# Kernel optimization log

Hardware: AMD Instinct MI355X
Metric: run time of the kernel (lower is better)

## Reference

```python
import jax, jax.numpy as jnp
import numpy as np
from functools import partial

B, T = 2048, 500
H1, H2, D_IN, D_FC, N_CLS = 128, 64, 1, 128, 4

def _lstm_scan(x, Wih, Whh, bih, bhh, hidden, return_seq):
    # x: (B, T, D). PyTorch gate order: i, f, g, o. Weights: (4H, D) / (4H, H).
    Bsz = x.shape[0]
    b = bih + bhh
    xg = jnp.einsum('btd,gd->btg', x, Wih) + b  # precompute input projections (B,T,4H)
    xg = jnp.swapaxes(xg, 0, 1)                 # (T,B,4H)
    h0 = jnp.zeros((Bsz, hidden), x.dtype)
    c0 = jnp.zeros((Bsz, hidden), x.dtype)

    def step(carry, gt):
        h, c = carry
        gates = gt + h @ Whh.T
        i, f, g, o = jnp.split(gates, 4, axis=-1)
        c = jax.nn.sigmoid(f) * c + jax.nn.sigmoid(i) * jnp.tanh(g)
        h = jax.nn.sigmoid(o) * jnp.tanh(c)
        return (h, c), (h if return_seq else None)

    (hT, _), hs = jax.lax.scan(step, (h0, c0), xg)
    if return_seq:
        return jnp.swapaxes(hs, 0, 1)  # (B,T,H)
    return hT  # (B,H)

def setup_inputs() -> dict:
    key = jax.random.key(0)
    ks = jax.random.split(key, 16)
    n = lambda k, shape: jax.random.normal(k, shape, dtype=jnp.float32) * 0.05
    return {
        'x': jax.random.normal(ks[0], (B, 1, T), dtype=jnp.float32),
        'Wp': n(ks[1], (H1, D_IN)), 'bp': n(ks[2], (H1,)),
        'Wih1': n(ks[3], (4 * H1, H1)), 'Whh1': n(ks[4], (4 * H1, H1)),
        'bih1': n(ks[5], (4 * H1,)), 'bhh1': n(ks[6], (4 * H1,)),
        'Wih2': n(ks[7], (4 * H2, H1)), 'Whh2': n(ks[8], (4 * H2, H2)),
        'bih2': n(ks[9], (4 * H2,)), 'bhh2': n(ks[10], (4 * H2,)),
        'W1': n(ks[11], (D_FC, H2)), 'b1': n(ks[12], (D_FC,)),
        'W2': n(ks[13], (N_CLS, D_FC)), 'b2': n(ks[14], (N_CLS,)),
    }

def reference(x, Wp, bp, Wih1, Whh1, bih1, bhh1, Wih2, Whh2, bih2, bhh2, W1, b1, W2, b2):
    # x: (B,1,T) -> (B,T,1)
    h = jnp.swapaxes(x, 1, 2)
    h = h @ Wp.T + bp                                         # (B,T,128)
    h = _lstm_scan(h, Wih1, Whh1, bih1, bhh1, H1, True)       # (B,T,128); dropout is identity in eval
    h = _lstm_scan(h, Wih2, Whh2, bih2, bhh2, H2, False)      # (B,64) == last-timestep output
    h = jax.nn.relu(h @ W1.T + b1)                            # (B,128)
    return h @ W2.T + b2                                      # (B,4)
```

## Files before the change

### kernel.cpp

```cpp
#include <hip/hip_runtime.h>


#define B_   2048
#define T_   500
#define BM   8
#define NBLK (B_ / BM)
#define NTHR 768

typedef __attribute__((ext_vector_type(8))) short bf16x8;
typedef __attribute__((ext_vector_type(4))) float f32x4;

#define LOG2E 1.44269504088896340736f

static __device__ __forceinline__ short f2bf(float f) {
  unsigned u = __builtin_bit_cast(unsigned, f);
  u = (u + 0x7fffu + ((u >> 16) & 1u)) >> 16;
  return (short)u;
}

static __device__ __forceinline__ float lstm_cell_s(float gi, float gf, float gg,
                                                    float go, float& c) {
  float Ei = __builtin_amdgcn_exp2f(-gi);
  float Eg = __builtin_amdgcn_exp2f(gg + gg);
  float Ef = __builtin_amdgcn_exp2f(-gf);
  float Eo = __builtin_amdgcn_exp2f(-go);
  float t12 = (1.f + Ei) * (1.f + Eg);
  float num = c * t12 + (Eg - 1.f) * (1.f + Ef);
  c = num * __builtin_amdgcn_rcpf((1.f + Ef) * t12);
  float Ec = __builtin_amdgcn_exp2f(2.88539008177792681472f * c);
  return (Ec - 1.f) * __builtin_amdgcn_rcpf((1.f + Eo) * (1.f + Ec));
}

__global__ __launch_bounds__(NTHR)
void lstm_fused(const float* __restrict__ X,
                const float* __restrict__ Wp,
                const float* __restrict__ bp,
                const float* __restrict__ Wih1,
                const float* __restrict__ Whh1,
                const float* __restrict__ bih1,
                const float* __restrict__ bhh1,
                const float* __restrict__ Wih2,
                const float* __restrict__ Whh2,
                const float* __restrict__ bih2,
                const float* __restrict__ bhh2,
                const float* __restrict__ W1,
                const float* __restrict__ b1,
                const float* __restrict__ W2,
                const float* __restrict__ b2,
                float* __restrict__ Out) {
  __shared__ __align__(16) short h1b[2][16][136];
  __shared__ __align__(16) short h2b[2][16][72];
  __shared__ __align__(16) short w2h[4][4][2][64][8];
  __shared__ float h2f[8][64];
  __shared__ float fc1s[8][132];

  const int tid = threadIdx.x;
  const int ln = tid & 63;
  const int wv = tid >> 6;
  const int cl = ln & 15;
  const int kg = ln >> 4;
  const int r0 = blockIdx.x * BM;
  const bool isL1 = (wv >= 4);
  const int w1 = wv - 4;

  bf16x8 Wreg[4][4];
  float uv[8];

  if (isL1) {
#pragma unroll
    for (int n = 0; n < 4; ++n) {
      const int R = n * 128 + 16 * w1 + cl;
      float u = 0.f, vv = bih1[R] + bhh1[R];
      const float4* Wi4 = (const float4*)(Wih1 + R * 128);
      const float4* Wp4 = (const float4*)Wp;
      const float4* bp4 = (const float4*)bp;
#pragma unroll 4
      for (int d = 0; d < 32; ++d) {
        float4 a = Wi4[d], pw = Wp4[d], qb = bp4[d];
        u  += a.x*pw.x + a.y*pw.y + a.z*pw.z + a.w*pw.w;
        vv += a.x*qb.x + a.y*qb.y + a.z*qb.z + a.w*qb.w;
      }
      uv[n] = u * LOG2E;
      uv[4 + n] = vv * LOG2E;
#pragma unroll
      for (int kf = 0; kf < 4; ++kf) {
        const float4* s4 = (const float4*)(Whh1 + R * 128 + kf * 32 + kg * 8);
        float4 a0 = s4[0], a1 = s4[1];
        bf16x8 fr;
        fr[0]=f2bf(a0.x*LOG2E); fr[1]=f2bf(a0.y*LOG2E);
        fr[2]=f2bf(a0.z*LOG2E); fr[3]=f2bf(a0.w*LOG2E);
        fr[4]=f2bf(a1.x*LOG2E); fr[5]=f2bf(a1.y*LOG2E);
        fr[6]=f2bf(a1.z*LOG2E); fr[7]=f2bf(a1.w*LOG2E);
        Wreg[n][kf] = fr;
      }
    }
  } else {
#pragma unroll
    for (int n = 0; n < 4; ++n) {
      const int R = n * 64 + 16 * wv + cl;
      uv[n] = (bih2[R] + bhh2[R]) * LOG2E;
#pragma unroll
      for (int kf = 0; kf < 4; ++kf) {
        const float4* s4 = (const float4*)(Wih2 + R * 128 + kf * 32 + kg * 8);
        float4 a0 = s4[0], a1 = s4[1];
        bf16x8 fr;
        fr[0]=f2bf(a0.x*LOG2E); fr[1]=f2bf(a0.y*LOG2E);
        fr[2]=f2bf(a0.z*LOG2E); fr[3]=f2bf(a0.w*LOG2E);
        fr[4]=f2bf(a1.x*LOG2E); fr[5]=f2bf(a1.y*LOG2E);
        fr[6]=f2bf(a1.z*LOG2E); fr[7]=f2bf(a1.w*LOG2E);
        Wreg[n][kf] = fr;
      }
#pragma unroll
      for (int kf = 0; kf < 2; ++kf) {
        const float4* s4 = (const float4*)(Whh2 + R * 64 + kf * 32 + kg * 8);
        float4 a0 = s4[0], a1 = s4[1];
        short* dst = &w2h[wv][n][kf][ln][0];
        dst[0]=f2bf(a0.x*LOG2E); dst[1]=f2bf(a0.y*LOG2E);
        dst[2]=f2bf(a0.z*LOG2E); dst[3]=f2bf(a0.w*LOG2E);
        dst[4]=f2bf(a1.x*LOG2E); dst[5]=f2bf(a1.y*LOG2E);
        dst[6]=f2bf(a1.z*LOG2E); dst[7]=f2bf(a1.w*LOG2E);
      }
    }
  }

  for (int i = tid; i < 2 * 16 * 136; i += NTHR) ((short*)h1b)[i] = 0;
  for (int i = tid; i < 2 * 16 * 72;  i += NTHR) ((short*)h2b)[i] = 0;
  __syncthreads();

  float c0 = 0.f, c1 = 0.f;
  const int rA = (kg < 2) ? kg * 4 : (kg - 2) * 4 + 2;
  const int rB = rA + 1;
  const int uu = 16 * (isL1 ? w1 : wv) + cl;

  float xr[4];
#pragma unroll
  for (int e = 0; e < 4; ++e)
    xr[e] = (isL1 && kg < 2) ? X[(size_t)(r0 + kg * 4 + e) * T_ + 0] : 0.f;

  for (int i = 0; i <= T_; ++i) {
    const int cur = i & 1, prv = cur ^ 1;

    if (isL1) {
      if (i < T_) {
        bf16x8 a1[4];
#pragma unroll
        for (int kf = 0; kf < 4; ++kf)
          a1[kf] = *(const bf16x8*)&h1b[prv][cl][kf * 32 + kg * 8];

        f32x4 acc[4];
#pragma unroll
        for (int n = 0; n < 4; ++n) {
#pragma unroll
          for (int e = 0; e < 4; ++e)
            acc[n][e] = xr[e] * uv[n] + uv[4 + n];
        }
        __builtin_amdgcn_s_setprio(1);
#pragma unroll
        for (int n = 0; n < 4; ++n)
#pragma unroll
          for (int kf = 0; kf < 4; ++kf)
            acc[n] = __builtin_amdgcn_mfma_f32_16x16x32_bf16(
                a1[kf], Wreg[n][kf], acc[n], 0, 0, 0);
        __builtin_amdgcn_s_setprio(0);

        if (kg < 2) {
          const int tn = (i + 1 < T_) ? i + 1 : T_ - 1;
#pragma unroll
          for (int e = 0; e < 4; ++e)
            xr[e] = X[(size_t)(r0 + kg * 4 + e) * T_ + tn];
        }

        float gA[4], gB[4];
#pragma unroll
        for (int n = 0; n < 4; ++n) {
          float s2 = __shfl_xor(acc[n][2], 32);
          float s3 = __shfl_xor(acc[n][3], 32);
          gA[n] = (kg < 2) ? acc[n][0] : s2;
          gB[n] = (kg < 2) ? acc[n][1] : s3;
        }
        float hA = lstm_cell_s(gA[0], gA[1], gA[2], gA[3], c0);
        float hB = lstm_cell_s(gB[0], gB[1], gB[2], gB[3], c1);
        h1b[cur][rA][uu] = f2bf(hA);
        h1b[cur][rB][uu] = f2bf(hB);
      }
    } else {
      if (i > 0) {
        bf16x8 a1[4], ag[2];
#pragma unroll
        for (int kf = 0; kf < 4; ++kf)
          a1[kf] = *(const bf16x8*)&h1b[prv][cl][kf * 32 + kg * 8];
#pragma unroll
        for (int kf = 0; kf < 2; ++kf)
          ag[kf] = *(const bf16x8*)&h2b[cur][cl][kf * 32 + kg * 8];

        f32x4 acc[4];
#pragma unroll
        for (int n = 0; n < 4; ++n)
          acc[n] = (f32x4){uv[n], uv[n], uv[n], uv[n]};
        __builtin_amdgcn_s_setprio(1);
#pragma unroll
        for (int n = 0; n < 4; ++n) {
          bf16x8 w0 = *(const bf16x8*)&w2h[wv][n][0][ln][0];
          bf16x8 w1f = *(const bf16x8*)&w2h[wv][n][1][ln][0];
          acc[n] = __builtin_amdgcn_mfma_f32_16x16x32_bf16(ag[0], w0, acc[n], 0, 0, 0);
          acc[n] = __builtin_amdgcn_mfma_f32_16x16x32_bf16(ag[1], w1f, acc[n], 0, 0, 0);
#pragma unroll
          for (int kf = 0; kf < 4; ++kf)
            acc[n] = __builtin_amdgcn_mfma_f32_16x16x32_bf16(
                a1[kf], Wreg[n][kf], acc[n], 0, 0, 0);
        }
        __builtin_amdgcn_s_setprio(0);

        float gA[4], gB[4];
#pragma unroll
        for (int n = 0; n < 4; ++n) {
          float s2 = __shfl_xor(acc[n][2], 32);
          float s3 = __shfl_xor(acc[n][3], 32);
          gA[n] = (kg < 2) ? acc[n][0] : s2;
          gB[n] = (kg < 2) ? acc[n][1] : s3;
        }
        float hA = lstm_cell_s(gA[0], gA[1], gA[2], gA[3], c0);
        float hB = lstm_cell_s(gB[0], gB[1], gB[2], gB[3], c1);
        h2b[prv][rA][uu] = f2bf(hA);
        h2b[prv][rB][uu] = f2bf(hB);
        if (i == T_) { h2f[rA][uu] = hA; h2f[rB][uu] = hB; }
      }
    }
    __syncthreads();
  }

  if (tid < 512) {
    const int u = tid & 127, r2 = tid >> 7;
    float a0 = b1[u], a1f = b1[u];
    for (int k = 0; k < 64; ++k) {
      float w = W1[u * 64 + k];
      a0  += h2f[r2 * 2 + 0][k] * w;
      a1f += h2f[r2 * 2 + 1][k] * w;
    }
    fc1s[r2 * 2 + 0][u] = fmaxf(a0, 0.f);
    fc1s[r2 * 2 + 1][u] = fmaxf(a1f, 0.f);
  }
  __syncthreads();
  if (tid < 32) {
    const int r = tid >> 2, cls = tid & 3;
    float a = b2[cls];
    for (int k = 0; k < 128; ++k) a += fc1s[r][k] * W2[cls * 128 + k];
    Out[(size_t)(r0 + r) * 4 + cls] = a;
  }
}

extern "C" void kernel_launch(void* const* d_in, const int* in_sizes, int n_in,
                              void* d_out, int out_size, void* d_ws, size_t ws_size,
                              hipStream_t stream) {
  const float* X    = (const float*)d_in[0];
  const float* Wp   = (const float*)d_in[1];
  const float* bp   = (const float*)d_in[2];
  const float* Wih1 = (const float*)d_in[3];
  const float* Whh1 = (const float*)d_in[4];
  const float* bih1 = (const float*)d_in[5];
  const float* bhh1 = (const float*)d_in[6];
  const float* Wih2 = (const float*)d_in[7];
  const float* Whh2 = (const float*)d_in[8];
  const float* bih2 = (const float*)d_in[9];
  const float* bhh2 = (const float*)d_in[10];
  const float* W1   = (const float*)d_in[11];
  const float* b1   = (const float*)d_in[12];
  const float* W2   = (const float*)d_in[13];
  const float* b2   = (const float*)d_in[14];
  float* Out = (float*)d_out;

  hipLaunchKernelGGL(lstm_fused, dim3(NBLK), dim3(NTHR), 0, stream,
                     X, Wp, bp, Wih1, Whh1, bih1, bhh1,
                     Wih2, Whh2, bih2, bhh2, W1, b1, W2, b2, Out);
}
```

Measured before the change: 534.8 us.

## Stage inputs in LDS, keep Whh2 in registers, peel loop edges, pack bf16 converts

Preloads the whole input sequence for the block's 8 rows into shared memory before the recurrence. This replaces the per-step global loads of X in layer-1 waves with one LDS vector read. Layer-2 recurrent weights move from LDS into registers, which removes two LDS reads per gate per step. The first and last timesteps are peeled out of the loop so the per-iteration branches disappear, and the two bf16 conversions are packed into one v_cvt_pk_bf16_f32. In exchange, register pressure rises in the layer-2 waves and the prologue pays a serialized global load into a 32 KB LDS buffer.

```diff
diff --git a/kernel.cpp b/kernel.cpp
--- a/kernel.cpp
+++ b/kernel.cpp
@@ -50,7 +50,7 @@
                 float* __restrict__ Out) {
   __shared__ __align__(16) short h1b[2][16][136];
   __shared__ __align__(16) short h2b[2][16][72];
-  __shared__ __align__(16) short w2h[4][4][2][64][8];
+  __shared__ __align__(16) float xs[T_][16];
   __shared__ float h2f[8][64];
   __shared__ float fc1s[8][132];
 
@@ -64,6 +64,7 @@
   const int w1 = wv - 4;
 
   bf16x8 Wreg[4][4];
+  bf16x8 W2h[4][2];
   float uv[8];
 
   if (isL1) {
@@ -114,17 +115,24 @@
       for (int kf = 0; kf < 2; ++kf) {
         const float4* s4 = (const float4*)(Whh2 + R * 64 + kf * 32 + kg * 8);
         float4 a0 = s4[0], a1 = s4[1];
-        short* dst = &w2h[wv][n][kf][ln][0];
-        dst[0]=f2bf(a0.x*LOG2E); dst[1]=f2bf(a0.y*LOG2E);
-        dst[2]=f2bf(a0.z*LOG2E); dst[3]=f2bf(a0.w*LOG2E);
-        dst[4]=f2bf(a1.x*LOG2E); dst[5]=f2bf(a1.y*LOG2E);
-        dst[6]=f2bf(a1.z*LOG2E); dst[7]=f2bf(a1.w*LOG2E);
+        bf16x8 fr;
+        fr[0]=f2bf(a0.x*LOG2E); fr[1]=f2bf(a0.y*LOG2E);
+        fr[2]=f2bf(a0.z*LOG2E); fr[3]=f2bf(a0.w*LOG2E);
+        fr[4]=f2bf(a1.x*LOG2E); fr[5]=f2bf(a1.y*LOG2E);
+        fr[6]=f2bf(a1.z*LOG2E); fr[7]=f2bf(a1.w*LOG2E);
+        W2h[n][kf] = fr;
       }
     }
   }
 
   for (int i = tid; i < 2 * 16 * 136; i += NTHR) ((short*)h1b)[i] = 0;
   for (int i = tid; i < 2 * 16 * 72;  i += NTHR) ((short*)h2b)[i] = 0;
+  for (int i = tid; i < T_ * 16; i += NTHR) ((float*)xs)[i] = 0.f;
+  __syncthreads();
+#pragma unroll
+  for (int r = 0; r < 8; ++r)
+    for (int t = tid; t < T_; t += NTHR)
+      xs[t][r] = X[(size_t)(r0 + r) * T_ + t];
   __syncthreads();
 
   float c0 = 0.f, c1 = 0.f;
@@ -132,102 +140,102 @@
   const int rB = rA + 1;
   const int uu = 16 * (isL1 ? w1 : wv) + cl;
 
-  float xr[4];
-#pragma unroll
-  for (int e = 0; e < 4; ++e)
-    xr[e] = (isL1 && kg < 2) ? X[(size_t)(r0 + kg * 4 + e) * T_ + 0] : 0.f;
-
-  for (int i = 0; i <= T_; ++i) {
+#define L1_STEP(i, cur, prv)                                                  \
+  {                                                                           \
+    bf16x8 a1[4];                                                             \
+    _Pragma("unroll")                                                         \
+    for (int kf = 0; kf < 4; ++kf)                                            \
+      a1[kf] = *(const bf16x8*)&h1b[prv][cl][kf * 32 + kg * 8];               \
+    f32x4 xr4 = *(const f32x4*)&xs[i][kg * 4];                                \
+    f32x4 acc[4];                                                             \
+    _Pragma("unroll")                                                         \
+    for (int n = 0; n < 4; ++n) {                                             \
+      _Pragma("unroll")                                                       \
+      for (int e = 0; e < 4; ++e)                                             \
+        acc[n][e] = xr4[e] * uv[n] + uv[4 + n];                               \
+    }                                                                         \
+    __builtin_amdgcn_s_setprio(1);                                            \
+    _Pragma("unroll")                                                         \
+    for (int n = 0; n < 4; ++n)                                               \
+      _Pragma("unroll")                                                       \
+      for (int kf = 0; kf < 4; ++kf)                                          \
+        acc[n] = __builtin_amdgcn_mfma_f32_16x16x32_bf16(                     \
+            a1[kf], Wreg[n][kf], acc[n], 0, 0, 0);                            \
+    __builtin_amdgcn_s_setprio(0);                                            \
+    float gA[4], gB[4];                                                       \
+    _Pragma("unroll")                                                         \
+    for (int n = 0; n < 4; ++n) {                                             \
+      float s2 = __shfl_xor(acc[n][2], 32);                                   \
+      float s3 = __shfl_xor(acc[n][3], 32);                                   \
+      gA[n] = (kg < 2) ? acc[n][0] : s2;                                      \
+      gB[n] = (kg < 2) ? acc[n][1] : s3;                                      \
+    }                                                                         \
+    float hA = lstm_cell_s(gA[0], gA[1], gA[2], gA[3], c0);                   \
+    float hB = lstm_cell_s(gB[0], gB[1], gB[2], gB[3], c1);                   \
+    unsigned pk;                                                              \
+    asm("v_cvt_pk_bf16_f32 %0, %1, %2" : "=v"(pk) : "v"(hA), "v"(hB));        \
+    h1b[cur][rA][uu] = (short)pk;                                             \
+    h1b[cur][rB][uu] = (short)(pk >> 16);                                     \
+  }
+
+#define L2_STEP(cur, prv, FINAL)                                              \
+  {                                                                           \
+    bf16x8 a1[4], ag[2];                                                      \
+    _Pragma("unroll")                                                         \
+    for (int kf = 0; kf < 4; ++kf)                                            \
+      a1[kf] = *(const bf16x8*)&h1b[prv][cl][kf * 32 + kg * 8];               \
+    _Pragma("unroll")                                                         \
+    for (int kf = 0; kf < 2; ++kf)                                            \
+      ag[kf] = *(const bf16x8*)&h2b[cur][cl][kf * 32 + kg * 8];               \
+    f32x4 acc[4];                                                             \
+    _Pragma("unroll")                                                         \
+    for (int n = 0; n < 4; ++n)                                               \
+      acc[n] = (f32x4){uv[n], uv[n], uv[n], uv[n]};                           \
+    __builtin_amdgcn_s_setprio(1);                                            \
+    _Pragma("unroll")                                                         \
+    for (int n = 0; n < 4; ++n) {                                             \
+      acc[n] = __builtin_amdgcn_mfma_f32_16x16x32_bf16(ag[0], W2h[n][0],      \
+                                                       acc[n], 0, 0, 0);      \
+      acc[n] = __builtin_amdgcn_mfma_f32_16x16x32_bf16(ag[1], W2h[n][1],      \
+                                                       acc[n], 0, 0, 0);      \
+      _Pragma("unroll")                                                       \
+      for (int kf = 0; kf < 4; ++kf)                                          \
+        acc[n] = __builtin_amdgcn_mfma_f32_16x16x32_bf16(                     \
+            a1[kf], Wreg[n][kf], acc[n], 0, 0, 0);                            \
+    }                                                                         \
+    __builtin_amdgcn_s_setprio(0);                                            \
+    float gA[4], gB[4];                                                       \
+    _Pragma("unroll")                                                         \
+    for (int n = 0; n < 4; ++n) {                                             \
+      float s2 = __shfl_xor(acc[n][2], 32);                                   \
+      float s3 = __shfl_xor(acc[n][3], 32);                                   \
+      gA[n] = (kg < 2) ? acc[n][0] : s2;                                      \
+      gB[n] = (kg < 2) ? acc[n][1] : s3;                                      \
+    }                                                                         \
+    float hA = lstm_cell_s(gA[0], gA[1], gA[2], gA[3], c0);                   \
+    float hB = lstm_cell_s(gB[0], gB[1], gB[2], gB[3], c1);                   \
+    unsigned pk;                                                              \
+    asm("v_cvt_pk_bf16_f32 %0, %1, %2" : "=v"(pk) : "v"(hA), "v"(hB));        \
+    h2b[prv][rA][uu] = (short)pk;                                             \
+    h2b[prv][rB][uu] = (short)(pk >> 16);                                     \
+    if (FINAL) { h2f[rA][uu] = hA; h2f[rB][uu] = hB; }                        \
+  }
+
+  if (isL1) L1_STEP(0, 0, 1);
+  __syncthreads();
+
+  for (int i = 1; i < T_; ++i) {
     const int cur = i & 1, prv = cur ^ 1;
-
     if (isL1) {
-      if (i < T_) {
-        bf16x8 a1[4];
-#pragma unroll
-        for (int kf = 0; kf < 4; ++kf)
-          a1[kf] = *(const bf16x8*)&h1b[prv][cl][kf * 32 + kg * 8];
-
-        f32x4 acc[4];
-#pragma unroll
-        for (int n = 0; n < 4; ++n) {
-#pragma unroll
-          for (int e = 0; e < 4; ++e)
-            acc[n][e] = xr[e] * uv[n] + uv[4 + n];
-        }
-        __builtin_amdgcn_s_setprio(1);
-#pragma unroll
-        for (int n = 0; n < 4; ++n)
-#pragma unroll
-          for (int kf = 0; kf < 4; ++kf)
-            acc[n] = __builtin_amdgcn_mfma_f32_16x16x32_bf16(
-                a1[kf], Wreg[n][kf], acc[n], 0, 0, 0);
-        __builtin_amdgcn_s_setprio(0);
-
-        if (kg < 2) {
-          const int tn = (i + 1 < T_) ? i + 1 : T_ - 1;
-#pragma unroll
-          for (int e = 0; e < 4; ++e)
-            xr[e] = X[(size_t)(r0 + kg * 4 + e) * T_ + tn];
-        }
-
-        float gA[4], gB[4];
-#pragma unroll
-        for (int n = 0; n < 4; ++n) {
-          float s2 = __shfl_xor(acc[n][2], 32);
-          float s3 = __shfl_xor(acc[n][3], 32);
-          gA[n] = (kg < 2) ? acc[n][0] : s2;
-          gB[n] = (kg < 2) ? acc[n][1] : s3;
-        }
-        float hA = lstm_cell_s(gA[0], gA[1], gA[2], gA[3], c0);
-        float hB = lstm_cell_s(gB[0], gB[1], gB[2], gB[3], c1);
-        h1b[cur][rA][uu] = f2bf(hA);
-        h1b[cur][rB][uu] = f2bf(hB);
-      }
+      L1_STEP(i, cur, prv);
     } else {
-      if (i > 0) {
-        bf16x8 a1[4], ag[2];
-#pragma unroll
-        for (int kf = 0; kf < 4; ++kf)
-          a1[kf] = *(const bf16x8*)&h1b[prv][cl][kf * 32 + kg * 8];
-#pragma unroll
-        for (int kf = 0; kf < 2; ++kf)
-          ag[kf] = *(const bf16x8*)&h2b[cur][cl][kf * 32 + kg * 8];
-
-        f32x4 acc[4];
-#pragma unroll
-        for (int n = 0; n < 4; ++n)
-          acc[n] = (f32x4){uv[n], uv[n], uv[n], uv[n]};
-        __builtin_amdgcn_s_setprio(1);
-#pragma unroll
-        for (int n = 0; n < 4; ++n) {
-          bf16x8 w0 = *(const bf16x8*)&w2h[wv][n][0][ln][0];
-          bf16x8 w1f = *(const bf16x8*)&w2h[wv][n][1][ln][0];
-          acc[n] = __builtin_amdgcn_mfma_f32_16x16x32_bf16(ag[0], w0, acc[n], 0, 0, 0);
-          acc[n] = __builtin_amdgcn_mfma_f32_16x16x32_bf16(ag[1], w1f, acc[n], 0, 0, 0);
-#pragma unroll
-          for (int kf = 0; kf < 4; ++kf)
-            acc[n] = __builtin_amdgcn_mfma_f32_16x16x32_bf16(
-                a1[kf], Wreg[n][kf], acc[n], 0, 0, 0);
-        }
-        __builtin_amdgcn_s_setprio(0);
-
-        float gA[4], gB[4];
-#pragma unroll
-        for (int n = 0; n < 4; ++n) {
-          float s2 = __shfl_xor(acc[n][2], 32);
-          float s3 = __shfl_xor(acc[n][3], 32);
-          gA[n] = (kg < 2) ? acc[n][0] : s2;
-          gB[n] = (kg < 2) ? acc[n][1] : s3;
-        }
-        float hA = lstm_cell_s(gA[0], gA[1], gA[2], gA[3], c0);
-        float hB = lstm_cell_s(gB[0], gB[1], gB[2], gB[3], c1);
-        h2b[prv][rA][uu] = f2bf(hA);
-        h2b[prv][rB][uu] = f2bf(hB);
-        if (i == T_) { h2f[rA][uu] = hA; h2f[rB][uu] = hB; }
-      }
+      L2_STEP(cur, prv, 0);
     }
     __syncthreads();
   }
+
+  if (!isL1) L2_STEP(0, 1, 1);
+  __syncthreads();
 
   if (tid < 512) {
     const int u = tid & 127, r2 = tid >> 7;
```

Result: slower. 553.2 us (+3.5%).
